# Kernel optimization log

Measured on AMD Instinct MI355X. Metric: run time of the kernel, lower is better.

The kernel has to match this reference:

```python
import jax, jax.numpy as jnp
import numpy as np

N_RAYS, N_SAMPLES = 65536, 128


def setup_inputs() -> dict:
    key = jax.random.key(0)
    k1, k2, k3 = jax.random.split(key, 3)
    # sample depths along each ray (unsorted; forward() sorts them)
    t = jax.random.uniform(k1, (N_RAYS, N_SAMPLES, 1), dtype=jnp.float32)
    # density (non-negative, as produced by a softplus/relu density head)
    sigma = jax.random.uniform(k2, (N_RAYS, N_SAMPLES, 1), dtype=jnp.float32)
    # per-sample RGB color in [0, 1]
    c = jax.random.uniform(k3, (N_RAYS, N_SAMPLES, 3), dtype=jnp.float32)
    return {"t": t, "sigma": sigma, "c": c}


def reference(t, sigma, c):
    # forward() sorts t along the sample axis before integration
    t = jnp.sort(t, axis=-2)
    # dt_i = t_{i+1} - t_i, padded with 0 at the end (infinite=False)
    dt = t[..., 1:, :] - t[..., :-1, :]
    dt = jnp.concatenate([dt, jnp.zeros_like(dt[..., :1, :])], axis=-2)
    sdt = sigma * dt                                   # [N, S, 1]
    # transmittance T_i = exp(-sum_{j<i} sigma_j dt_j); exclusive prefix sum
    Ti = jnp.exp(-jnp.cumsum(sdt, axis=-2))[..., :-1, :]
    Ti = jnp.concatenate([jnp.ones_like(Ti[..., :1, :]), Ti], axis=-2)
    alpha = 1.0 - jnp.exp(-sdt)
    wi = Ti * alpha                                    # compositing weights [N, S, 1]
    color = (wi * c).sum(axis=-2)                      # [N, 3]
    depth = (wi * t).sum(axis=-2)                      # [N, 1]
    return color, depth, wi
```

## Files before the change

kernel.cpp:

```cpp
#include <hip/hip_runtime.h>


#define CEX(a,b) { float mn_=fminf(v[a],v[b]); v[b]=fmaxf(v[a],v[b]); v[a]=mn_; }

#define CROSS_REV(mask, lowbit) { \
  float w_[8]; \
  _Pragma("unroll") for (int r_=0;r_<8;++r_) w_[r_]=__shfl_xor(v[7-r_], (mask)); \
  const bool lo_ = (gl & (lowbit)) == 0; \
  _Pragma("unroll") for (int r_=0;r_<8;++r_) \
    v[r_] = lo_ ? fminf(v[r_],w_[r_]) : fmaxf(v[r_],w_[r_]); }

#define CROSS(mask, lowbit) { \
  float w_[8]; \
  _Pragma("unroll") for (int r_=0;r_<8;++r_) w_[r_]=__shfl_xor(v[r_], (mask)); \
  const bool lo_ = (gl & (lowbit)) == 0; \
  _Pragma("unroll") for (int r_=0;r_<8;++r_) \
    v[r_] = lo_ ? fminf(v[r_],w_[r_]) : fmaxf(v[r_],w_[r_]); }

#define INLANE8() { CEX(0,4) CEX(1,5) CEX(2,6) CEX(3,7) \
                    CEX(0,2) CEX(1,3) CEX(4,6) CEX(5,7) \
                    CEX(0,1) CEX(2,3) CEX(4,5) CEX(6,7) }

__global__ __launch_bounds__(256) void nerf_render_kernel(
    const float* __restrict__ t,
    const float* __restrict__ sigma,
    const float* __restrict__ c,
    float* __restrict__ out,
    int n_rays) {
  const int tid  = threadIdx.x;
  const int lane = tid & 63;
  const int gl   = lane & 15;
  const int ray  = blockIdx.x * 16 + (tid >> 4);
  if (ray >= n_rays) return;

  const float4* tb = (const float4*)(t + (size_t)ray * 128 + gl * 8);
  float v[8];
  { float4 a = tb[0], b = tb[1];
    v[0]=a.x; v[1]=a.y; v[2]=a.z; v[3]=a.w;
    v[4]=b.x; v[5]=b.y; v[6]=b.z; v[7]=b.w; }

  CEX(0,1) CEX(2,3) CEX(4,5) CEX(6,7)
  CEX(0,2) CEX(1,3) CEX(4,6) CEX(5,7)
  CEX(1,2) CEX(5,6)
  CEX(0,4) CEX(1,5) CEX(2,6) CEX(3,7)
  CEX(2,4) CEX(3,5)
  CEX(1,2) CEX(3,4) CEX(5,6)

  CROSS_REV(1, 1)  INLANE8()
  CROSS_REV(3, 2)  CROSS(1, 1)  INLANE8()
  CROSS_REV(7, 4)  CROSS(2, 2)  CROSS(1, 1)  INLANE8()
  CROSS_REV(15, 8) CROSS(4, 4)  CROSS(2, 2)  CROSS(1, 1)  INLANE8()

  const float nxt = __shfl(v[0], (lane + 1) & 63);
  float dt[8];
#pragma unroll
  for (int r = 0; r < 7; ++r) dt[r] = v[r + 1] - v[r];
  dt[7] = (gl == 15) ? 0.0f : (nxt - v[7]);

  const float4* sb = (const float4*)(sigma + (size_t)ray * 128 + gl * 8);
  float sdt[8];
  { float4 a = sb[0], b = sb[1];
    sdt[0]=a.x*dt[0]; sdt[1]=a.y*dt[1]; sdt[2]=a.z*dt[2]; sdt[3]=a.w*dt[3];
    sdt[4]=b.x*dt[4]; sdt[5]=b.y*dt[5]; sdt[6]=b.z*dt[6]; sdt[7]=b.w*dt[7]; }

  float p[8];
  p[0] = sdt[0];
#pragma unroll
  for (int r = 1; r < 8; ++r) p[r] = p[r - 1] + sdt[r];
  float s = p[7];
#pragma unroll
  for (int off = 1; off < 16; off <<= 1) {
    const float u = __shfl_up(s, off);
    if (gl >= off) s += u;
  }
  const float excl = s - p[7];

  float wi[8];
  float Eprev = __expf(-excl);
#pragma unroll
  for (int r = 0; r < 8; ++r) {
    const float Er = __expf(-(excl + p[r]));
    wi[r] = Eprev - Er;
    Eprev = Er;
  }

  float carr[24];
  { const float4* cb = (const float4*)(c + (size_t)ray * 384 + gl * 24);
#pragma unroll
    for (int q = 0; q < 6; ++q) *(float4*)&carr[q * 4] = cb[q]; }
  float pr = 0.f, pg = 0.f, pb = 0.f, pd = 0.f;
#pragma unroll
  for (int r = 0; r < 8; ++r) {
    pr += wi[r] * carr[3 * r + 0];
    pg += wi[r] * carr[3 * r + 1];
    pb += wi[r] * carr[3 * r + 2];
    pd += wi[r] * v[r];
  }

#pragma unroll
  for (int m = 8; m >= 1; m >>= 1) {
    pr += __shfl_xor(pr, m);
    pg += __shfl_xor(pg, m);
    pb += __shfl_xor(pb, m);
    pd += __shfl_xor(pd, m);
  }

  float* wo = out + (size_t)n_rays * 4 + (size_t)ray * 128 + gl * 8;
  *(float4*)(wo)     = make_float4(wi[0], wi[1], wi[2], wi[3]);
  *(float4*)(wo + 4) = make_float4(wi[4], wi[5], wi[6], wi[7]);
  if (gl == 0) {
    out[(size_t)ray * 3 + 0] = pr;
    out[(size_t)ray * 3 + 1] = pg;
    out[(size_t)ray * 3 + 2] = pb;
    out[(size_t)n_rays * 3 + ray] = pd;
  }
}

extern "C" void kernel_launch(void* const* d_in, const int* in_sizes, int n_in,
                              void* d_out, int out_size, void* d_ws, size_t ws_size,
                              hipStream_t stream) {
  const float* t     = (const float*)d_in[0];
  const float* sigma = (const float*)d_in[1];
  const float* c     = (const float*)d_in[2];
  float* out = (float*)d_out;
  const int n_rays = in_sizes[0] / 128;
  const int blocks = (n_rays + 15) / 16;
  nerf_render_kernel<<<blocks, 256, 0, stream>>>(t, sigma, c, out, n_rays);
}
```

Baseline: 34.57 us.

## Process each ray with 8 lanes of 16 samples instead of 16 lanes of 8

Changes the per-ray work split from 16 lanes holding 8 samples each to 8 lanes holding 16 samples each, so a block now covers 32 rays. The bitonic sort does more work in registers (sort two 8-element runs, then merge to 16) and needs one fewer cross-lane merge stage, with fewer shuffles in the scan and reductions. The trade-off is higher register pressure (48-float color array, 16-wide sort buffers), which may lower occupancy on a memory-bound kernel.

```diff
diff --git a/kernel.cpp b/kernel.cpp
--- a/kernel.cpp
+++ b/kernel.cpp
@@ -3,23 +3,42 @@
 
 #define CEX(a,b) { float mn_=fminf(v[a],v[b]); v[b]=fmaxf(v[a],v[b]); v[a]=mn_; }
 
+#define SORT8(B) \
+  CEX(B+0,B+1) CEX(B+2,B+3) CEX(B+4,B+5) CEX(B+6,B+7) \
+  CEX(B+0,B+2) CEX(B+1,B+3) CEX(B+4,B+6) CEX(B+5,B+7) \
+  CEX(B+1,B+2) CEX(B+5,B+6) \
+  CEX(B+0,B+4) CEX(B+1,B+5) CEX(B+2,B+6) CEX(B+3,B+7) \
+  CEX(B+2,B+4) CEX(B+3,B+5) \
+  CEX(B+1,B+2) CEX(B+3,B+4) CEX(B+5,B+6)
+
+#define MERGE8(B) \
+  CEX(B+0,B+4) CEX(B+1,B+5) CEX(B+2,B+6) CEX(B+3,B+7) \
+  CEX(B+0,B+2) CEX(B+1,B+3) CEX(B+4,B+6) CEX(B+5,B+7) \
+  CEX(B+0,B+1) CEX(B+2,B+3) CEX(B+4,B+5) CEX(B+6,B+7)
+
+#define MERGE16_FROM_8 \
+  CEX(0,15) CEX(1,14) CEX(2,13) CEX(3,12) CEX(4,11) CEX(5,10) CEX(6,9) CEX(7,8) \
+  MERGE8(0) MERGE8(8)
+
+#define INLANE16 \
+  CEX(0,8) CEX(1,9) CEX(2,10) CEX(3,11) CEX(4,12) CEX(5,13) CEX(6,14) CEX(7,15) \
+  CEX(0,4) CEX(1,5) CEX(2,6) CEX(3,7) CEX(8,12) CEX(9,13) CEX(10,14) CEX(11,15) \
+  CEX(0,2) CEX(1,3) CEX(4,6) CEX(5,7) CEX(8,10) CEX(9,11) CEX(12,14) CEX(13,15) \
+  CEX(0,1) CEX(2,3) CEX(4,5) CEX(6,7) CEX(8,9) CEX(10,11) CEX(12,13) CEX(14,15)
+
 #define CROSS_REV(mask, lowbit) { \
-  float w_[8]; \
-  _Pragma("unroll") for (int r_=0;r_<8;++r_) w_[r_]=__shfl_xor(v[7-r_], (mask)); \
+  float w_[16]; \
+  _Pragma("unroll") for (int r_=0;r_<16;++r_) w_[r_]=__shfl_xor(v[15-r_], (mask)); \
   const bool lo_ = (gl & (lowbit)) == 0; \
-  _Pragma("unroll") for (int r_=0;r_<8;++r_) \
+  _Pragma("unroll") for (int r_=0;r_<16;++r_) \
     v[r_] = lo_ ? fminf(v[r_],w_[r_]) : fmaxf(v[r_],w_[r_]); }
 
 #define CROSS(mask, lowbit) { \
-  float w_[8]; \
-  _Pragma("unroll") for (int r_=0;r_<8;++r_) w_[r_]=__shfl_xor(v[r_], (mask)); \
+  float w_[16]; \
+  _Pragma("unroll") for (int r_=0;r_<16;++r_) w_[r_]=__shfl_xor(v[r_], (mask)); \
   const bool lo_ = (gl & (lowbit)) == 0; \
-  _Pragma("unroll") for (int r_=0;r_<8;++r_) \
+  _Pragma("unroll") for (int r_=0;r_<16;++r_) \
     v[r_] = lo_ ? fminf(v[r_],w_[r_]) : fmaxf(v[r_],w_[r_]); }
-
-#define INLANE8() { CEX(0,4) CEX(1,5) CEX(2,6) CEX(3,7) \
-                    CEX(0,2) CEX(1,3) CEX(4,6) CEX(5,7) \
-                    CEX(0,1) CEX(2,3) CEX(4,5) CEX(6,7) }
 
 __global__ __launch_bounds__(256) void nerf_render_kernel(
     const float* __restrict__ t,
@@ -29,85 +48,91 @@
     int n_rays) {
   const int tid  = threadIdx.x;
   const int lane = tid & 63;
-  const int gl   = lane & 15;
-  const int ray  = blockIdx.x * 16 + (tid >> 4);
+  const int gl   = lane & 7;
+  const int ray  = blockIdx.x * 32 + (tid >> 3);
   if (ray >= n_rays) return;
 
-  const float4* tb = (const float4*)(t + (size_t)ray * 128 + gl * 8);
-  float v[8];
-  { float4 a = tb[0], b = tb[1];
-    v[0]=a.x; v[1]=a.y; v[2]=a.z; v[3]=a.w;
-    v[4]=b.x; v[5]=b.y; v[6]=b.z; v[7]=b.w; }
+  const float4* tb = (const float4*)(t + (size_t)ray * 128 + gl * 16);
+  float v[16];
+#pragma unroll
+  for (int q = 0; q < 4; ++q) {
+    const float4 a = tb[q];
+    v[4*q+0]=a.x; v[4*q+1]=a.y; v[4*q+2]=a.z; v[4*q+3]=a.w;
+  }
 
-  CEX(0,1) CEX(2,3) CEX(4,5) CEX(6,7)
-  CEX(0,2) CEX(1,3) CEX(4,6) CEX(5,7)
-  CEX(1,2) CEX(5,6)
-  CEX(0,4) CEX(1,5) CEX(2,6) CEX(3,7)
-  CEX(2,4) CEX(3,5)
-  CEX(1,2) CEX(3,4) CEX(5,6)
+  SORT8(0) SORT8(8) MERGE16_FROM_8
 
-  CROSS_REV(1, 1)  INLANE8()
-  CROSS_REV(3, 2)  CROSS(1, 1)  INLANE8()
-  CROSS_REV(7, 4)  CROSS(2, 2)  CROSS(1, 1)  INLANE8()
-  CROSS_REV(15, 8) CROSS(4, 4)  CROSS(2, 2)  CROSS(1, 1)  INLANE8()
+  CROSS_REV(1, 1)                          INLANE16
+  CROSS_REV(3, 2) CROSS(1, 1)              INLANE16
+  CROSS_REV(7, 4) CROSS(2, 2) CROSS(1, 1)  INLANE16
 
   const float nxt = __shfl(v[0], (lane + 1) & 63);
-  float dt[8];
+  float dt[16];
 #pragma unroll
-  for (int r = 0; r < 7; ++r) dt[r] = v[r + 1] - v[r];
-  dt[7] = (gl == 15) ? 0.0f : (nxt - v[7]);
+  for (int r = 0; r < 15; ++r) dt[r] = v[r + 1] - v[r];
+  dt[15] = (gl == 7) ? 0.0f : (nxt - v[15]);
 
-  const float4* sb = (const float4*)(sigma + (size_t)ray * 128 + gl * 8);
-  float sdt[8];
-  { float4 a = sb[0], b = sb[1];
-    sdt[0]=a.x*dt[0]; sdt[1]=a.y*dt[1]; sdt[2]=a.z*dt[2]; sdt[3]=a.w*dt[3];
-    sdt[4]=b.x*dt[4]; sdt[5]=b.y*dt[5]; sdt[6]=b.z*dt[6]; sdt[7]=b.w*dt[7]; }
+  const float4* sb = (const float4*)(sigma + (size_t)ray * 128 + gl * 16);
+  float p[16];
+  {
+    float run = 0.f;
+#pragma unroll
+    for (int q = 0; q < 4; ++q) {
+      const float4 a = sb[q];
+      run += a.x * dt[4*q+0]; p[4*q+0] = run;
+      run += a.y * dt[4*q+1]; p[4*q+1] = run;
+      run += a.z * dt[4*q+2]; p[4*q+2] = run;
+      run += a.w * dt[4*q+3]; p[4*q+3] = run;
+    }
+  }
 
-  float p[8];
-  p[0] = sdt[0];
+  float s = p[15];
 #pragma unroll
-  for (int r = 1; r < 8; ++r) p[r] = p[r - 1] + sdt[r];
-  float s = p[7];
-#pragma unroll
-  for (int off = 1; off < 16; off <<= 1) {
+  for (int off = 1; off < 8; off <<= 1) {
     const float u = __shfl_up(s, off);
     if (gl >= off) s += u;
   }
-  const float excl = s - p[7];
+  const float excl = s - p[15];
 
-  float wi[8];
-  float Eprev = __expf(-excl);
+  float wi[16];
+  {
+    float Eprev = __expf(-excl);
 #pragma unroll
-  for (int r = 0; r < 8; ++r) {
-    const float Er = __expf(-(excl + p[r]));
-    wi[r] = Eprev - Er;
-    Eprev = Er;
+    for (int r = 0; r < 16; ++r) {
+      const float Er = __expf(-(excl + p[r]));
+      wi[r] = Eprev - Er;
+      Eprev = Er;
+    }
   }
 
-  float carr[24];
-  { const float4* cb = (const float4*)(c + (size_t)ray * 384 + gl * 24);
+  float pr = 0.f, pg = 0.f, pb = 0.f, pd = 0.f;
+  {
+    const float4* cb = (const float4*)(c + (size_t)ray * 384 + gl * 48);
+    float carr[48];
 #pragma unroll
-    for (int q = 0; q < 6; ++q) *(float4*)&carr[q * 4] = cb[q]; }
-  float pr = 0.f, pg = 0.f, pb = 0.f, pd = 0.f;
+    for (int q = 0; q < 12; ++q) *(float4*)&carr[q * 4] = cb[q];
 #pragma unroll
-  for (int r = 0; r < 8; ++r) {
-    pr += wi[r] * carr[3 * r + 0];
-    pg += wi[r] * carr[3 * r + 1];
-    pb += wi[r] * carr[3 * r + 2];
-    pd += wi[r] * v[r];
+    for (int r = 0; r < 16; ++r) {
+      pr += wi[r] * carr[3 * r + 0];
+      pg += wi[r] * carr[3 * r + 1];
+      pb += wi[r] * carr[3 * r + 2];
+      pd += wi[r] * v[r];
+    }
   }
 
 #pragma unroll
-  for (int m = 8; m >= 1; m >>= 1) {
+  for (int m = 4; m >= 1; m >>= 1) {
     pr += __shfl_xor(pr, m);
     pg += __shfl_xor(pg, m);
     pb += __shfl_xor(pb, m);
     pd += __shfl_xor(pd, m);
   }
 
-  float* wo = out + (size_t)n_rays * 4 + (size_t)ray * 128 + gl * 8;
-  *(float4*)(wo)     = make_float4(wi[0], wi[1], wi[2], wi[3]);
-  *(float4*)(wo + 4) = make_float4(wi[4], wi[5], wi[6], wi[7]);
+  float* wo = out + (size_t)n_rays * 4 + (size_t)ray * 128 + gl * 16;
+#pragma unroll
+  for (int q = 0; q < 4; ++q)
+    *(float4*)(wo + 4 * q) =
+        make_float4(wi[4*q+0], wi[4*q+1], wi[4*q+2], wi[4*q+3]);
   if (gl == 0) {
     out[(size_t)ray * 3 + 0] = pr;
     out[(size_t)ray * 3 + 1] = pg;
@@ -124,6 +149,6 @@
   const float* c     = (const float*)d_in[2];
   float* out = (float*)d_out;
   const int n_rays = in_sizes[0] / 128;
-  const int blocks = (n_rays + 15) / 16;
+  const int blocks = (n_rays + 31) / 32;
   nerf_render_kernel<<<blocks, 256, 0, stream>>>(t, sigma, c, out, n_rays);
 }
```

Measured after the change: 50.87 us. +47.2%, slower.
